# Kernel tuning notes

Hardware: AMD Instinct MI355X
Metric: run time of the kernel (lower is better)

Reference implementation:

```python
import jax, jax.numpy as jnp
import numpy as np

B, T, IN, H, OUT = 16384, 200, 9, 64, 3


def setup_inputs() -> dict:
    key = jax.random.key(0)
    ks = jax.random.split(key, 12)
    s_in, s_h = 1.0 / np.sqrt(H), 1.0 / np.sqrt(H)  # torch LSTMCell init scale = 1/sqrt(hidden)
    u = lambda k, shape: jax.random.uniform(k, shape, jnp.float32, -s_h, s_h)
    return {
        "x": jax.random.normal(ks[0], (B, T, IN), jnp.float32),
        "W_ih1": u(ks[1], (4 * H, IN)),
        "W_hh1": u(ks[2], (4 * H, H)),
        "b_ih1": u(ks[3], (4 * H,)),
        "b_hh1": u(ks[4], (4 * H,)),
        "W_ih2": u(ks[5], (4 * H, H)),
        "W_hh2": u(ks[6], (4 * H, H)),
        "b_ih2": u(ks[7], (4 * H,)),
        "b_hh2": u(ks[8], (4 * H,)),
        "W_out": u(ks[9], (OUT, H)),
        "b_out": u(ks[10], (OUT,)),
    }


def _lstm_cell(x, h, c, W_ih, W_hh, b_ih, b_hh):
    # PyTorch gate order: i, f, g, o
    gates = x @ W_ih.T + b_ih + h @ W_hh.T + b_hh  # [B, 4H]
    i, f, g, o = jnp.split(gates, 4, axis=-1)
    i, f, o = jax.nn.sigmoid(i), jax.nn.sigmoid(f), jax.nn.sigmoid(o)
    g = jnp.tanh(g)
    c_new = f * c + i * g
    h_new = o * jnp.tanh(c_new)
    return h_new, c_new


def reference(x, W_ih1, W_hh1, b_ih1, b_hh1, W_ih2, W_hh2, b_ih2, b_hh2, W_out, b_out):
    batch = x.shape[0]
    hdim = W_hh1.shape[1]
    zeros = jnp.zeros((batch, hdim), x.dtype)
    init = (zeros, zeros, zeros, zeros)  # h1, c1, h2, c2

    def step(carry, x_t):
        h1, c1, h2, c2 = carry
        h1, c1 = _lstm_cell(x_t, h1, c1, W_ih1, W_hh1, b_ih1, b_hh1)
        h2, c2 = _lstm_cell(h1, h2, c2, W_ih2, W_hh2, b_ih2, b_hh2)
        return (h1, c1, h2, c2), None

    (h1, c1, h2, c2), _ = jax.lax.scan(step, init, jnp.swapaxes(x, 0, 1))  # scan over time
    out = h2 @ W_out.T + b_out  # [B, OUT]
    return out[:, None, :]  # [B, 1, OUT]
```

## Files before the change

### kernel.cpp

```cpp
#include <hip/hip_runtime.h>
#include <hip/hip_bf16.h>


#define B_TOT   16384
#define T_STEPS 200
#define IN_DIM  9
#define HDIM    64

#define PK1_OFF 0
#define PK2_OFF 24576
#define BSUM_HALF_OFF 57344
#define PACK_W_TOT 57344
#define PACK_TOT (PACK_W_TOT + 512)

#define L2E     1.44269504089f
#define TWOL2E  2.88539008178f

typedef _Float16 half8  __attribute__((ext_vector_type(8)));
typedef _Float16 half4v __attribute__((ext_vector_type(4)));
typedef float    f32x4  __attribute__((ext_vector_type(4)));
typedef float    f4u    __attribute__((ext_vector_type(4), aligned(4)));

__global__ void pack_kernel(const float* __restrict__ Wih1, const float* __restrict__ Whh1,
                            const float* __restrict__ bih1, const float* __restrict__ bhh1,
                            const float* __restrict__ Wih2, const float* __restrict__ Whh2,
                            const float* __restrict__ bih2, const float* __restrict__ bhh2,
                            float* __restrict__ ws) {
    int e = blockIdx.x * 256 + threadIdx.x;
    if (e >= PACK_TOT) return;
    _Float16* wh = (_Float16*)ws;
    float* bptr = (float*)(wh + BSUM_HALF_OFF);
    auto gscale = [](int q) -> float {
        int gt = q >> 6;
        return (gt == 2) ? (-2.0f * L2E) : -L2E;
    };
    if (e < PK2_OFF) {
        int j = e & 7, lane = (e >> 3) & 63, nt = (e >> 9) & 15, c = e >> 13;
        int k = c * 32 + 4 * (lane >> 4) + (j & 3) + 16 * (j >> 2);
        int q = nt * 16 + (lane & 15);
        float v = 0.0f;
        if (k < 64)      v = Whh1[q * 64 + k];
        else if (k < 73) v = Wih1[q * 9 + (k - 64)];
        wh[e] = (_Float16)(v * gscale(q));
    } else if (e < PACK_W_TOT) {
        int e2 = e - PK2_OFF;
        int j = e2 & 7, lane = (e2 >> 3) & 63, nt = (e2 >> 9) & 15, c = e2 >> 13;
        int k = c * 32 + 4 * (lane >> 4) + (j & 3) + 16 * (j >> 2);
        int q = nt * 16 + (lane & 15);
        float v = (k < 64) ? Wih2[q * 64 + k] : Whh2[q * 64 + (k - 64)];
        wh[e] = (_Float16)(v * gscale(q));
    } else if (e < PACK_W_TOT + 256) {
        int q = e - PACK_W_TOT;
        bptr[q] = (bih1[q] + bhh1[q]) * gscale(q);
    } else {
        int q = e - PACK_W_TOT - 256;
        bptr[256 + q] = (bih2[q] + bhh2[q]) * gscale(q);
    }
}

__global__ __launch_bounds__(256, 2) void lstm_mfma(
    const float* __restrict__ x,
    const float* __restrict__ ws_f,
    const float* __restrict__ Wout,
    const float* __restrict__ bout,
    float* __restrict__ out)
{
    const int tid  = threadIdx.x;
    const int lane = tid & 63;
    const int w    = __builtin_amdgcn_readfirstlane(tid >> 6);
    const int l15  = lane & 15;
    const int l4   = lane >> 4;

    const _Float16* wh  = (const _Float16*)ws_f;
    const _Float16* pk1 = wh + PK1_OFF;
    const _Float16* pk2 = wh + PK2_OFF;
    const float* bsum   = (const float*)(wh + BSUM_HALF_OFF);

    __shared__ _Float16 h1P[2][16][72], h2P[2][16][72];
    __shared__ _Float16 h1Q[2][16][72], h2Q[2][16][72];
    __shared__ _Float16 xwP[2][8][4][16][4], xwQ[2][8][4][16][4];

    for (int i = tid; i < 2 * 16 * 72; i += 256) {
        (&h1P[0][0][0])[i] = (_Float16)0.0f; (&h2P[0][0][0])[i] = (_Float16)0.0f;
        (&h1Q[0][0][0])[i] = (_Float16)0.0f; (&h2Q[0][0][0])[i] = (_Float16)0.0f;
    }
    for (int i = tid; i < 2 * 8 * 4 * 16 * 4; i += 256) {
        (&xwP[0][0][0][0][0])[i] = (_Float16)0.0f;
        (&xwQ[0][0][0][0][0])[i] = (_Float16)0.0f;
    }

    const int bbase = blockIdx.x * 32;

    const int b_ = tid & 15, z_ = tid >> 4;
    const int s0_ = (z_ * 11) >> 5, q0_ = z_ - 3 * s0_;
    const bool act1 = (z_ < 8);
    const int pz1 = z_ + 16;
    const int s1_ = (pz1 * 11) >> 5, q1_ = pz1 - 3 * s1_;
    const float* xbP = x + (long)(bbase + b_) * (T_STEPS * IN_DIM);
    const float* xbQ = x + (long)(bbase + 16 + b_) * (T_STEPS * IN_DIM);

    f4u pfPA = {0.f,0.f,0.f,0.f}, pfPB = {0.f,0.f,0.f,0.f};
    f4u pfQA = {0.f,0.f,0.f,0.f}, pfQB = {0.f,0.f,0.f,0.f};

    auto fetch_t = [&](const float* xb, f4u& A, f4u& B, int wb) {
        int t0 = wb + s0_; if (t0 > T_STEPS - 1) t0 = T_STEPS - 1;
        const float* p0 = xb + t0 * IN_DIM + 4 * q0_;
        if (q0_ < 2) A = *(const f4u*)p0; else A[0] = p0[0];
        if (act1) {
            int t1 = wb + s1_; if (t1 > T_STEPS - 1) t1 = T_STEPS - 1;
            const float* p1 = xb + t1 * IN_DIM + 4 * q1_;
            if (q1_ < 2) B = *(const f4u*)p1; else B[0] = p1[0];
        }
    };
    auto store_t = [&](_Float16 (*xw)[8][4][16][4], f4u A, f4u B, int buf) {
        if (q0_ == 2) { A[1] = 0.f; A[2] = 0.f; A[3] = 0.f; }
        half4v hv;
        hv[0] = (_Float16)A[0]; hv[1] = (_Float16)A[1];
        hv[2] = (_Float16)A[2]; hv[3] = (_Float16)A[3];
        *(half4v*)&xw[buf][s0_][q0_][b_][0] = hv;
        if (act1) {
            if (q1_ == 2) { B[1] = 0.f; B[2] = 0.f; B[3] = 0.f; }
            half4v hw;
            hw[0] = (_Float16)B[0]; hw[1] = (_Float16)B[1];
            hw[2] = (_Float16)B[2]; hw[3] = (_Float16)B[3];
            *(half4v*)&xw[buf][s1_][q1_][b_][0] = hw;
        }
    };
    auto read_ax = [&](const _Float16 (*xw)[8][4][16][4], int tt) -> half8 {
        half4v xq = *(const half4v*)&xw[(tt >> 3) & 1][tt & 7][l4][l15][0];
        return __builtin_shufflevector(xq, xq, 0, 1, 2, 3, 0, 1, 2, 3);
    };

    half8 bw1_00, bw1_01, bw1_02, bw1_03;
    half8 bw1_10, bw1_11, bw1_12, bw1_13;
    half8 bw1_20, bw1_21, bw1_22, bw1_23;
    half8 bw2_00, bw2_01, bw2_02, bw2_03;
    half8 bw2_10, bw2_11, bw2_12, bw2_13;
    half8 bw2_20, bw2_21, bw2_22, bw2_23;
    half8 bw2_30, bw2_31, bw2_32, bw2_33;
    {
        #define LD1(c,g) *(const half8*)(pk1 + (((c * 16) + (w + 4 * g)) * 64 + lane) * 8)
        #define LD2(c,g) *(const half8*)(pk2 + (((c * 16) + (w + 4 * g)) * 64 + lane) * 8)
        bw1_00 = LD1(0,0); bw1_01 = LD1(0,1); bw1_02 = LD1(0,2); bw1_03 = LD1(0,3);
        bw1_10 = LD1(1,0); bw1_11 = LD1(1,1); bw1_12 = LD1(1,2); bw1_13 = LD1(1,3);
        bw1_20 = LD1(2,0); bw1_21 = LD1(2,1); bw1_22 = LD1(2,2); bw1_23 = LD1(2,3);
        bw2_00 = LD2(0,0); bw2_01 = LD2(0,1); bw2_02 = LD2(0,2); bw2_03 = LD2(0,3);
        bw2_10 = LD2(1,0); bw2_11 = LD2(1,1); bw2_12 = LD2(1,2); bw2_13 = LD2(1,3);
        bw2_20 = LD2(2,0); bw2_21 = LD2(2,1); bw2_22 = LD2(2,2); bw2_23 = LD2(2,3);
        bw2_30 = LD2(3,0); bw2_31 = LD2(3,1); bw2_32 = LD2(3,2); bw2_33 = LD2(3,3);
        #undef LD1
        #undef LD2
    }

    float bias1[4], bias2[4];
    #pragma unroll
    for (int g = 0; g < 4; ++g) {
        bias1[g] = bsum[(w + 4 * g) * 16 + l15];
        bias2[g] = bsum[256 + (w + 4 * g) * 16 + l15];
    }

    const int hpos = ((w >> 1) << 5) + 8 * (l15 >> 2) + (l15 & 3) + ((w & 1) << 2);

    f32x4 c1P = {0.f,0.f,0.f,0.f}, c2P = {0.f,0.f,0.f,0.f};
    f32x4 c1Q = {0.f,0.f,0.f,0.f}, c2Q = {0.f,0.f,0.f,0.f};

    auto cell_update = [&](f32x4* G, f32x4& cs, _Float16* hb) {
        float num[4], den[4], eo4[4], d2[4], hs4[4];
        #pragma unroll
        for (int r = 0; r < 4; ++r) {
            float ei = __builtin_amdgcn_exp2f(G[0][r]);
            float ef = __builtin_amdgcn_exp2f(G[1][r]);
            float eg = __builtin_amdgcn_exp2f(G[2][r]);
            eo4[r]   = __builtin_amdgcn_exp2f(G[3][r]);
            float ai = 1.0f + ei, af = 1.0f + ef, ag = 1.0f + eg;
            float gm = 1.0f - eg;
            float pp = ai * ag;
            num[r] = __builtin_fmaf(gm, af, cs[r] * pp);
            den[r] = af * pp;
        }
        float s01 = den[0] * den[1], s23 = den[2] * den[3];
        float Pinv = __builtin_amdgcn_rcpf(s01 * s23);
        float r01 = Pinv * s23, r23 = Pinv * s01;
        float inv[4] = {r01 * den[1], r01 * den[0], r23 * den[3], r23 * den[2]};
        #pragma unroll
        for (int r = 0; r < 4; ++r) {
            float cc = num[r] * inv[r];
            cs[r] = cc;
            float z  = cc * TWOL2E;
            int   zi = __float_as_int(z);
            float ec = __builtin_amdgcn_exp2f(__int_as_float(zi | (int)0x80000000));
            float tm = 1.0f - ec;
            d2[r] = (1.0f + eo4[r]) * (1.0f + ec);
            hs4[r] = __int_as_float(__float_as_int(tm) ^ (zi & (int)0x80000000));
        }
        float t01 = d2[0] * d2[1], t23 = d2[2] * d2[3];
        float Qinv = __builtin_amdgcn_rcpf(t01 * t23);
        float q01 = Qinv * t23, q23 = Qinv * t01;
        float jnv[4] = {q01 * d2[1], q01 * d2[0], q23 * d2[3], q23 * d2[2]};
        #pragma unroll
        for (int r = 0; r < 4; ++r)
            hb[(4 * l4 + r) * 72 + hpos] = (_Float16)(hs4[r] * jnv[r]);
    };

    auto initb = [&](f32x4* A, const float* b) {
        #pragma unroll
        for (int g = 0; g < 4; ++g) A[g] = (f32x4){b[g], b[g], b[g], b[g]};
    };
    auto L2C = [&](f32x4* D, half8 u0, half8 u1, half8 v0, half8 v1) {
        D[0] = __builtin_amdgcn_mfma_f32_16x16x32_f16(u0, bw2_00, D[0], 0, 0, 0);
        D[1] = __builtin_amdgcn_mfma_f32_16x16x32_f16(u0, bw2_01, D[1], 0, 0, 0);
        D[2] = __builtin_amdgcn_mfma_f32_16x16x32_f16(u0, bw2_02, D[2], 0, 0, 0);
        D[3] = __builtin_amdgcn_mfma_f32_16x16x32_f16(u0, bw2_03, D[3], 0, 0, 0);
        D[0] = __builtin_amdgcn_mfma_f32_16x16x32_f16(u1, bw2_10, D[0], 0, 0, 0);
        D[1] = __builtin_amdgcn_mfma_f32_16x16x32_f16(u1, bw2_11, D[1], 0, 0, 0);
        D[2] = __builtin_amdgcn_mfma_f32_16x16x32_f16(u1, bw2_12, D[2], 0, 0, 0);
        D[3] = __builtin_amdgcn_mfma_f32_16x16x32_f16(u1, bw2_13, D[3], 0, 0, 0);
        D[0] = __builtin_amdgcn_mfma_f32_16x16x32_f16(v0, bw2_20, D[0], 0, 0, 0);
        D[1] = __builtin_amdgcn_mfma_f32_16x16x32_f16(v0, bw2_21, D[1], 0, 0, 0);
        D[2] = __builtin_amdgcn_mfma_f32_16x16x32_f16(v0, bw2_22, D[2], 0, 0, 0);
        D[3] = __builtin_amdgcn_mfma_f32_16x16x32_f16(v0, bw2_23, D[3], 0, 0, 0);
        D[0] = __builtin_amdgcn_mfma_f32_16x16x32_f16(v1, bw2_30, D[0], 0, 0, 0);
        D[1] = __builtin_amdgcn_mfma_f32_16x16x32_f16(v1, bw2_31, D[1], 0, 0, 0);
        D[2] = __builtin_amdgcn_mfma_f32_16x16x32_f16(v1, bw2_32, D[2], 0, 0, 0);
        D[3] = __builtin_amdgcn_mfma_f32_16x16x32_f16(v1, bw2_33, D[3], 0, 0, 0);
    };
    auto L1C = [&](f32x4* C, half8 u0, half8 u1, half8 axm) {
        C[0] = __builtin_amdgcn_mfma_f32_16x16x32_f16(u0, bw1_00, C[0], 0, 0, 0);
        C[1] = __builtin_amdgcn_mfma_f32_16x16x32_f16(u0, bw1_01, C[1], 0, 0, 0);
        C[2] = __builtin_amdgcn_mfma_f32_16x16x32_f16(u0, bw1_02, C[2], 0, 0, 0);
        C[3] = __builtin_amdgcn_mfma_f32_16x16x32_f16(u0, bw1_03, C[3], 0, 0, 0);
        C[0] = __builtin_amdgcn_mfma_f32_16x16x32_f16(u1, bw1_10, C[0], 0, 0, 0);
        C[1] = __builtin_amdgcn_mfma_f32_16x16x32_f16(u1, bw1_11, C[1], 0, 0, 0);
        C[2] = __builtin_amdgcn_mfma_f32_16x16x32_f16(u1, bw1_12, C[2], 0, 0, 0);
        C[3] = __builtin_amdgcn_mfma_f32_16x16x32_f16(u1, bw1_13, C[3], 0, 0, 0);
        C[0] = __builtin_amdgcn_mfma_f32_16x16x32_f16(axm, bw1_20, C[0], 0, 0, 0);
        C[1] = __builtin_amdgcn_mfma_f32_16x16x32_f16(axm, bw1_21, C[1], 0, 0, 0);
        C[2] = __builtin_amdgcn_mfma_f32_16x16x32_f16(axm, bw1_22, C[2], 0, 0, 0);
        C[3] = __builtin_amdgcn_mfma_f32_16x16x32_f16(axm, bw1_23, C[3], 0, 0, 0);
    };

    #define PIN_ALL() do {                                                      \
        asm volatile("" :                                                       \
            "+v"(bw1_00), "+v"(bw1_01), "+v"(bw1_02), "+v"(bw1_03),             \
            "+v"(bw1_10), "+v"(bw1_11), "+v"(bw1_12), "+v"(bw1_13),             \
            "+v"(bw1_20), "+v"(bw1_21), "+v"(bw1_22), "+v"(bw1_23));            \
        asm volatile("" :                                                       \
            "+v"(bw2_00), "+v"(bw2_01), "+v"(bw2_02), "+v"(bw2_03),             \
            "+v"(bw2_10), "+v"(bw2_11), "+v"(bw2_12), "+v"(bw2_13),             \
            "+v"(bw2_20), "+v"(bw2_21), "+v"(bw2_22), "+v"(bw2_23),             \
            "+v"(bw2_30), "+v"(bw2_31), "+v"(bw2_32), "+v"(bw2_33),             \
            "+v"(bias1[0]), "+v"(bias1[1]), "+v"(bias1[2]), "+v"(bias1[3]),     \
            "+v"(bias2[0]), "+v"(bias2[1]), "+v"(bias2[2]), "+v"(bias2[3]));    \
    } while (0)

    fetch_t(xbP, pfPA, pfPB, 0);
    fetch_t(xbQ, pfQA, pfQB, 0);
    __syncthreads();
    store_t(xwP, pfPA, pfPB, 0);
    store_t(xwQ, pfQA, pfQB, 0);
    fetch_t(xbP, pfPA, pfPB, 8);
    fetch_t(xbQ, pfQA, pfQB, 8);
    __syncthreads();

    f32x4 CP[4], CQ[4];
    {
        half8 ax0 = read_ax(xwP, 0);
        initb(CP, bias1);
        CP[0] = __builtin_amdgcn_mfma_f32_16x16x32_f16(ax0, bw1_20, CP[0], 0, 0, 0);
        CP[1] = __builtin_amdgcn_mfma_f32_16x16x32_f16(ax0, bw1_21, CP[1], 0, 0, 0);
        CP[2] = __builtin_amdgcn_mfma_f32_16x16x32_f16(ax0, bw1_22, CP[2], 0, 0, 0);
        CP[3] = __builtin_amdgcn_mfma_f32_16x16x32_f16(ax0, bw1_23, CP[3], 0, 0, 0);
        half8 ax1 = read_ax(xwQ, 0);
        initb(CQ, bias1);
        CQ[0] = __builtin_amdgcn_mfma_f32_16x16x32_f16(ax1, bw1_20, CQ[0], 0, 0, 0);
        CQ[1] = __builtin_amdgcn_mfma_f32_16x16x32_f16(ax1, bw1_21, CQ[1], 0, 0, 0);
        CQ[2] = __builtin_amdgcn_mfma_f32_16x16x32_f16(ax1, bw1_22, CQ[2], 0, 0, 0);
        CQ[3] = __builtin_amdgcn_mfma_f32_16x16x32_f16(ax1, bw1_23, CQ[3], 0, 0, 0);
    }

    for (int t = 0; t < T_STEPS; t += 2) {
        PIN_ALL();
        cell_update(CP, c1P, &h1P[1][0][0]);
        cell_update(CQ, c1Q, &h1Q[1][0][0]);
        if ((t & 7) == 0) {
            int nb = ((t >> 3) + 1) & 1;
            store_t(xwP, pfPA, pfPB, nb);
            store_t(xwQ, pfQA, pfQB, nb);
            fetch_t(xbP, pfPA, pfPB, t + 16);
            fetch_t(xbQ, pfQA, pfQB, t + 16);
        }
        __syncthreads();
        __builtin_amdgcn_s_setprio(1);
        {
            half8 u0 = *(const half8*)&h1P[1][l15][ 0 + 8 * l4];
            half8 u1 = *(const half8*)&h1P[1][l15][32 + 8 * l4];
            half8 v0 = *(const half8*)&h2P[0][l15][ 0 + 8 * l4];
            half8 v1 = *(const half8*)&h2P[0][l15][32 + 8 * l4];
            half8 axm = read_ax(xwP, t + 1);
            f32x4 D[4]; initb(D, bias2);
            L2C(D, u0, u1, v0, v1);
            initb(CP, bias1);
            L1C(CP, u0, u1, axm);
            cell_update(D, c2P, &h2P[1][0][0]);
        }
        {
            half8 u0 = *(const half8*)&h1Q[1][l15][ 0 + 8 * l4];
            half8 u1 = *(const half8*)&h1Q[1][l15][32 + 8 * l4];
            half8 v0 = *(const half8*)&h2Q[0][l15][ 0 + 8 * l4];
            half8 v1 = *(const half8*)&h2Q[0][l15][32 + 8 * l4];
            half8 axm = read_ax(xwQ, t + 1);
            f32x4 D[4]; initb(D, bias2);
            L2C(D, u0, u1, v0, v1);
            initb(CQ, bias1);
            L1C(CQ, u0, u1, axm);
            cell_update(D, c2Q, &h2Q[1][0][0]);
        }
        __builtin_amdgcn_s_setprio(0);

        PIN_ALL();
        cell_update(CP, c1P, &h1P[0][0][0]);
        cell_update(CQ, c1Q, &h1Q[0][0][0]);
        __syncthreads();
        __builtin_amdgcn_s_setprio(1);
        {
            half8 u0 = *(const half8*)&h1P[0][l15][ 0 + 8 * l4];
            half8 u1 = *(const half8*)&h1P[0][l15][32 + 8 * l4];
            half8 v0 = *(const half8*)&h2P[1][l15][ 0 + 8 * l4];
            half8 v1 = *(const half8*)&h2P[1][l15][32 + 8 * l4];
            half8 axm = read_ax(xwP, t + 2);
            f32x4 D[4]; initb(D, bias2);
            L2C(D, u0, u1, v0, v1);
            initb(CP, bias1);
            L1C(CP, u0, u1, axm);
            cell_update(D, c2P, &h2P[0][0][0]);
        }
        {
            half8 u0 = *(const half8*)&h1Q[0][l15][ 0 + 8 * l4];
            half8 u1 = *(const half8*)&h1Q[0][l15][32 + 8 * l4];
            half8 v0 = *(const half8*)&h2Q[1][l15][ 0 + 8 * l4];
            half8 v1 = *(const half8*)&h2Q[1][l15][32 + 8 * l4];
            half8 axm = read_ax(xwQ, t + 2);
            f32x4 D[4]; initb(D, bias2);
            L2C(D, u0, u1, v0, v1);
            initb(CQ, bias1);
            L1C(CQ, u0, u1, axm);
            cell_update(D, c2Q, &h2Q[0][0][0]);
        }
        __builtin_amdgcn_s_setprio(0);
    }
    __syncthreads();

    if (tid < 96) {
        int bl = tid / 3, o = tid - bl * 3;
        const _Float16* src = (bl < 16) ? &h2P[0][bl][0] : &h2Q[0][bl - 16][0];
        float acc = bout[o];
        #pragma unroll 8
        for (int pos = 0; pos < HDIM; ++pos) {
            int sub = pos & 31;
            int j = (pos >> 5) * 32 + (((sub >> 2) & 1) << 4) + ((sub >> 3) << 2) + (sub & 3);
            acc = __builtin_fmaf(Wout[o * 64 + j], (float)src[pos], acc);
        }
        out[(bbase + bl) * 3 + o] = acc;
    }
    #undef PIN_ALL
}

extern "C" void kernel_launch(void* const* d_in, const int* in_sizes, int n_in,
                              void* d_out, int out_size, void* d_ws, size_t ws_size,
                              hipStream_t stream) {
    const float* x     = (const float*)d_in[0];
    const float* Wih1  = (const float*)d_in[1];
    const float* Whh1  = (const float*)d_in[2];
    const float* bih1  = (const float*)d_in[3];
    const float* bhh1  = (const float*)d_in[4];
    const float* Wih2  = (const float*)d_in[5];
    const float* Whh2  = (const float*)d_in[6];
    const float* bih2  = (const float*)d_in[7];
    const float* bhh2  = (const float*)d_in[8];
    const float* Wout  = (const float*)d_in[9];
    const float* bout  = (const float*)d_in[10];
    float* ws  = (float*)d_ws;
    float* out = (float*)d_out;

    pack_kernel<<<(PACK_TOT + 255) / 256, 256, 0, stream>>>(
        Wih1, Whh1, bih1, bhh1, Wih2, Whh2, bih2, bhh2, ws);

    lstm_mfma<<<B_TOT / 32, 256, 0, stream>>>(x, ws, Wout, bout, out);
}
```

Baseline: 557.4 us.

## Load x per step directly into registers instead of staging through LDS

Removes the shared-memory staging buffers for the input sequence, along with their cooperative fetch and store every eight steps. Each lane now prefetches its own x slice from global memory one step ahead and builds the MFMA A operand in registers. This drops LDS traffic and extra shuffle work, but adds a small global load on every step with only one step of latency hiding. The s_setprio hints around the MFMA phases are also removed, and the per-step body is refactored into a tile_phase helper.

```diff
diff --git a/kernel.cpp b/kernel.cpp
--- a/kernel.cpp
+++ b/kernel.cpp
@@ -17,7 +17,6 @@
 #define TWOL2E  2.88539008178f
 
 typedef _Float16 half8  __attribute__((ext_vector_type(8)));
-typedef _Float16 half4v __attribute__((ext_vector_type(4)));
 typedef float    f32x4  __attribute__((ext_vector_type(4)));
 typedef float    f4u    __attribute__((ext_vector_type(4), aligned(4)));
 
@@ -78,57 +77,30 @@
 
     __shared__ _Float16 h1P[2][16][72], h2P[2][16][72];
     __shared__ _Float16 h1Q[2][16][72], h2Q[2][16][72];
-    __shared__ _Float16 xwP[2][8][4][16][4], xwQ[2][8][4][16][4];
 
     for (int i = tid; i < 2 * 16 * 72; i += 256) {
         (&h1P[0][0][0])[i] = (_Float16)0.0f; (&h2P[0][0][0])[i] = (_Float16)0.0f;
         (&h1Q[0][0][0])[i] = (_Float16)0.0f; (&h2Q[0][0][0])[i] = (_Float16)0.0f;
     }
-    for (int i = tid; i < 2 * 8 * 4 * 16 * 4; i += 256) {
-        (&xwP[0][0][0][0][0])[i] = (_Float16)0.0f;
-        (&xwQ[0][0][0][0][0])[i] = (_Float16)0.0f;
-    }
 
     const int bbase = blockIdx.x * 32;
-
-    const int b_ = tid & 15, z_ = tid >> 4;
-    const int s0_ = (z_ * 11) >> 5, q0_ = z_ - 3 * s0_;
-    const bool act1 = (z_ < 8);
-    const int pz1 = z_ + 16;
-    const int s1_ = (pz1 * 11) >> 5, q1_ = pz1 - 3 * s1_;
-    const float* xbP = x + (long)(bbase + b_) * (T_STEPS * IN_DIM);
-    const float* xbQ = x + (long)(bbase + 16 + b_) * (T_STEPS * IN_DIM);
-
-    f4u pfPA = {0.f,0.f,0.f,0.f}, pfPB = {0.f,0.f,0.f,0.f};
-    f4u pfQA = {0.f,0.f,0.f,0.f}, pfQB = {0.f,0.f,0.f,0.f};
-
-    auto fetch_t = [&](const float* xb, f4u& A, f4u& B, int wb) {
-        int t0 = wb + s0_; if (t0 > T_STEPS - 1) t0 = T_STEPS - 1;
-        const float* p0 = xb + t0 * IN_DIM + 4 * q0_;
-        if (q0_ < 2) A = *(const f4u*)p0; else A[0] = p0[0];
-        if (act1) {
-            int t1 = wb + s1_; if (t1 > T_STEPS - 1) t1 = T_STEPS - 1;
-            const float* p1 = xb + t1 * IN_DIM + 4 * q1_;
-            if (q1_ < 2) B = *(const f4u*)p1; else B[0] = p1[0];
-        }
-    };
-    auto store_t = [&](_Float16 (*xw)[8][4][16][4], f4u A, f4u B, int buf) {
-        if (q0_ == 2) { A[1] = 0.f; A[2] = 0.f; A[3] = 0.f; }
-        half4v hv;
-        hv[0] = (_Float16)A[0]; hv[1] = (_Float16)A[1];
-        hv[2] = (_Float16)A[2]; hv[3] = (_Float16)A[3];
-        *(half4v*)&xw[buf][s0_][q0_][b_][0] = hv;
-        if (act1) {
-            if (q1_ == 2) { B[1] = 0.f; B[2] = 0.f; B[3] = 0.f; }
-            half4v hw;
-            hw[0] = (_Float16)B[0]; hw[1] = (_Float16)B[1];
-            hw[2] = (_Float16)B[2]; hw[3] = (_Float16)B[3];
-            *(half4v*)&xw[buf][s1_][q1_][b_][0] = hw;
-        }
-    };
-    auto read_ax = [&](const _Float16 (*xw)[8][4][16][4], int tt) -> half8 {
-        half4v xq = *(const half4v*)&xw[(tt >> 3) & 1][tt & 7][l4][l15][0];
-        return __builtin_shufflevector(xq, xq, 0, 1, 2, 3, 0, 1, 2, 3);
+    const float* xbP = x + (long)(bbase + l15) * (T_STEPS * IN_DIM);
+    const float* xbQ = x + (long)(bbase + 16 + l15) * (T_STEPS * IN_DIM);
+
+    f4u  cxP = {0.f,0.f,0.f,0.f}, cxQ = {0.f,0.f,0.f,0.f};
+    float cx8P = 0.0f, cx8Q = 0.0f;
+    auto prefetch_tile = [&](const float* xb, f4u& cx, float& cx8, int tt) {
+        const float* xp = xb + tt * IN_DIM;
+        if (l4 < 2)       cx  = *(const f4u*)(xp + 4 * l4);
+        else if (l4 == 2) cx8 = xp[8];
+    };
+    auto build_ax2 = [&](const f4u& cx, float cx8) -> half8 {
+        half8 ax;
+        float e0 = (l4 == 2) ? cx8 : cx[0];
+        ax[0] = (_Float16)e0;    ax[1] = (_Float16)cx[1];
+        ax[2] = (_Float16)cx[2]; ax[3] = (_Float16)cx[3];
+        ax[4] = ax[5] = ax[6] = ax[7] = (_Float16)0.0f;
+        return ax;
     };
 
     half8 bw1_00, bw1_01, bw1_02, bw1_03;
@@ -206,7 +178,15 @@
         #pragma unroll
         for (int g = 0; g < 4; ++g) A[g] = (f32x4){b[g], b[g], b[g], b[g]};
     };
-    auto L2C = [&](f32x4* D, half8 u0, half8 u1, half8 v0, half8 v1) {
+
+    auto tile_phase = [&](f32x4* Cacc, f32x4& cs2,
+                          const _Float16* h1w, const _Float16* h2r,
+                          _Float16* h2w, half8 axn) {
+        half8 u0 = *(const half8*)(h1w + l15 * 72 +  0 + 8 * l4);
+        half8 u1 = *(const half8*)(h1w + l15 * 72 + 32 + 8 * l4);
+        half8 v0 = *(const half8*)(h2r + l15 * 72 +  0 + 8 * l4);
+        half8 v1 = *(const half8*)(h2r + l15 * 72 + 32 + 8 * l4);
+        f32x4 D[4]; initb(D, bias2);
         D[0] = __builtin_amdgcn_mfma_f32_16x16x32_f16(u0, bw2_00, D[0], 0, 0, 0);
         D[1] = __builtin_amdgcn_mfma_f32_16x16x32_f16(u0, bw2_01, D[1], 0, 0, 0);
         D[2] = __builtin_amdgcn_mfma_f32_16x16x32_f16(u0, bw2_02, D[2], 0, 0, 0);
@@ -223,20 +203,20 @@
         D[1] = __builtin_amdgcn_mfma_f32_16x16x32_f16(v1, bw2_31, D[1], 0, 0, 0);
         D[2] = __builtin_amdgcn_mfma_f32_16x16x32_f16(v1, bw2_32, D[2], 0, 0, 0);
         D[3] = __builtin_amdgcn_mfma_f32_16x16x32_f16(v1, bw2_33, D[3], 0, 0, 0);
-    };
-    auto L1C = [&](f32x4* C, half8 u0, half8 u1, half8 axm) {
-        C[0] = __builtin_amdgcn_mfma_f32_16x16x32_f16(u0, bw1_00, C[0], 0, 0, 0);
-        C[1] = __builtin_amdgcn_mfma_f32_16x16x32_f16(u0, bw1_01, C[1], 0, 0, 0);
-        C[2] = __builtin_amdgcn_mfma_f32_16x16x32_f16(u0, bw1_02, C[2], 0, 0, 0);
-        C[3] = __builtin_amdgcn_mfma_f32_16x16x32_f16(u0, bw1_03, C[3], 0, 0, 0);
-        C[0] = __builtin_amdgcn_mfma_f32_16x16x32_f16(u1, bw1_10, C[0], 0, 0, 0);
-        C[1] = __builtin_amdgcn_mfma_f32_16x16x32_f16(u1, bw1_11, C[1], 0, 0, 0);
-        C[2] = __builtin_amdgcn_mfma_f32_16x16x32_f16(u1, bw1_12, C[2], 0, 0, 0);
-        C[3] = __builtin_amdgcn_mfma_f32_16x16x32_f16(u1, bw1_13, C[3], 0, 0, 0);
-        C[0] = __builtin_amdgcn_mfma_f32_16x16x32_f16(axm, bw1_20, C[0], 0, 0, 0);
-        C[1] = __builtin_amdgcn_mfma_f32_16x16x32_f16(axm, bw1_21, C[1], 0, 0, 0);
-        C[2] = __builtin_amdgcn_mfma_f32_16x16x32_f16(axm, bw1_22, C[2], 0, 0, 0);
-        C[3] = __builtin_amdgcn_mfma_f32_16x16x32_f16(axm, bw1_23, C[3], 0, 0, 0);
+        initb(Cacc, bias1);
+        Cacc[0] = __builtin_amdgcn_mfma_f32_16x16x32_f16(u0, bw1_00, Cacc[0], 0, 0, 0);
+        Cacc[1] = __builtin_amdgcn_mfma_f32_16x16x32_f16(u0, bw1_01, Cacc[1], 0, 0, 0);
+        Cacc[2] = __builtin_amdgcn_mfma_f32_16x16x32_f16(u0, bw1_02, Cacc[2], 0, 0, 0);
+        Cacc[3] = __builtin_amdgcn_mfma_f32_16x16x32_f16(u0, bw1_03, Cacc[3], 0, 0, 0);
+        Cacc[0] = __builtin_amdgcn_mfma_f32_16x16x32_f16(u1, bw1_10, Cacc[0], 0, 0, 0);
+        Cacc[1] = __builtin_amdgcn_mfma_f32_16x16x32_f16(u1, bw1_11, Cacc[1], 0, 0, 0);
+        Cacc[2] = __builtin_amdgcn_mfma_f32_16x16x32_f16(u1, bw1_12, Cacc[2], 0, 0, 0);
+        Cacc[3] = __builtin_amdgcn_mfma_f32_16x16x32_f16(u1, bw1_13, Cacc[3], 0, 0, 0);
+        Cacc[0] = __builtin_amdgcn_mfma_f32_16x16x32_f16(axn, bw1_20, Cacc[0], 0, 0, 0);
+        Cacc[1] = __builtin_amdgcn_mfma_f32_16x16x32_f16(axn, bw1_21, Cacc[1], 0, 0, 0);
+        Cacc[2] = __builtin_amdgcn_mfma_f32_16x16x32_f16(axn, bw1_22, Cacc[2], 0, 0, 0);
+        Cacc[3] = __builtin_amdgcn_mfma_f32_16x16x32_f16(axn, bw1_23, Cacc[3], 0, 0, 0);
+        cell_update(D, cs2, h2w);
     };
 
     #define PIN_ALL() do {                                                      \
@@ -253,100 +233,49 @@
             "+v"(bias2[0]), "+v"(bias2[1]), "+v"(bias2[2]), "+v"(bias2[3]));    \
     } while (0)
 
-    fetch_t(xbP, pfPA, pfPB, 0);
-    fetch_t(xbQ, pfQA, pfQB, 0);
-    __syncthreads();
-    store_t(xwP, pfPA, pfPB, 0);
-    store_t(xwQ, pfQA, pfQB, 0);
-    fetch_t(xbP, pfPA, pfPB, 8);
-    fetch_t(xbQ, pfQA, pfQB, 8);
-    __syncthreads();
-
+    prefetch_tile(xbP, cxP, cx8P, 0);
+    prefetch_tile(xbQ, cxQ, cx8Q, 0);
     f32x4 CP[4], CQ[4];
     {
-        half8 ax0 = read_ax(xwP, 0);
+        half8 ax0 = build_ax2(cxP, cx8P);
         initb(CP, bias1);
         CP[0] = __builtin_amdgcn_mfma_f32_16x16x32_f16(ax0, bw1_20, CP[0], 0, 0, 0);
         CP[1] = __builtin_amdgcn_mfma_f32_16x16x32_f16(ax0, bw1_21, CP[1], 0, 0, 0);
         CP[2] = __builtin_amdgcn_mfma_f32_16x16x32_f16(ax0, bw1_22, CP[2], 0, 0, 0);
         CP[3] = __builtin_amdgcn_mfma_f32_16x16x32_f16(ax0, bw1_23, CP[3], 0, 0, 0);
-        half8 ax1 = read_ax(xwQ, 0);
+        half8 ax1 = build_ax2(cxQ, cx8Q);
         initb(CQ, bias1);
         CQ[0] = __builtin_amdgcn_mfma_f32_16x16x32_f16(ax1, bw1_20, CQ[0], 0, 0, 0);
         CQ[1] = __builtin_amdgcn_mfma_f32_16x16x32_f16(ax1, bw1_21, CQ[1], 0, 0, 0);
         CQ[2] = __builtin_amdgcn_mfma_f32_16x16x32_f16(ax1, bw1_22, CQ[2], 0, 0, 0);
         CQ[3] = __builtin_amdgcn_mfma_f32_16x16x32_f16(ax1, bw1_23, CQ[3], 0, 0, 0);
     }
+    prefetch_tile(xbP, cxP, cx8P, 1);
+    prefetch_tile(xbQ, cxQ, cx8Q, 1);
+    __syncthreads();
 
     for (int t = 0; t < T_STEPS; t += 2) {
         PIN_ALL();
+        half8 axP = build_ax2(cxP, cx8P);
+        half8 axQ = build_ax2(cxQ, cx8Q);
+        prefetch_tile(xbP, cxP, cx8P, t + 2 < T_STEPS ? t + 2 : T_STEPS - 1);
+        prefetch_tile(xbQ, cxQ, cx8Q, t + 2 < T_STEPS ? t + 2 : T_STEPS - 1);
         cell_update(CP, c1P, &h1P[1][0][0]);
         cell_update(CQ, c1Q, &h1Q[1][0][0]);
-        if ((t & 7) == 0) {
-            int nb = ((t >> 3) + 1) & 1;
-            store_t(xwP, pfPA, pfPB, nb);
-            store_t(xwQ, pfQA, pfQB, nb);
-            fetch_t(xbP, pfPA, pfPB, t + 16);
-            fetch_t(xbQ, pfQA, pfQB, t + 16);
-        }
         __syncthreads();
-        __builtin_amdgcn_s_setprio(1);
-        {
-            half8 u0 = *(const half8*)&h1P[1][l15][ 0 + 8 * l4];
-            half8 u1 = *(const half8*)&h1P[1][l15][32 + 8 * l4];
-            half8 v0 = *(const half8*)&h2P[0][l15][ 0 + 8 * l4];
-            half8 v1 = *(const half8*)&h2P[0][l15][32 + 8 * l4];
-            half8 axm = read_ax(xwP, t + 1);
-            f32x4 D[4]; initb(D, bias2);
-            L2C(D, u0, u1, v0, v1);
-            initb(CP, bias1);
-            L1C(CP, u0, u1, axm);
-            cell_update(D, c2P, &h2P[1][0][0]);
-        }
-        {
-            half8 u0 = *(const half8*)&h1Q[1][l15][ 0 + 8 * l4];
-            half8 u1 = *(const half8*)&h1Q[1][l15][32 + 8 * l4];
-            half8 v0 = *(const half8*)&h2Q[0][l15][ 0 + 8 * l4];
-            half8 v1 = *(const half8*)&h2Q[0][l15][32 + 8 * l4];
-            half8 axm = read_ax(xwQ, t + 1);
-            f32x4 D[4]; initb(D, bias2);
-            L2C(D, u0, u1, v0, v1);
-            initb(CQ, bias1);
-            L1C(CQ, u0, u1, axm);
-            cell_update(D, c2Q, &h2Q[1][0][0]);
-        }
-        __builtin_amdgcn_s_setprio(0);
+        tile_phase(CP, c2P, &h1P[1][0][0], &h2P[0][0][0], &h2P[1][0][0], axP);
+        tile_phase(CQ, c2Q, &h1Q[1][0][0], &h2Q[0][0][0], &h2Q[1][0][0], axQ);
 
         PIN_ALL();
+        half8 bxP = build_ax2(cxP, cx8P);
+        half8 bxQ = build_ax2(cxQ, cx8Q);
+        prefetch_tile(xbP, cxP, cx8P, t + 3 < T_STEPS ? t + 3 : T_STEPS - 1);
+        prefetch_tile(xbQ, cxQ, cx8Q, t + 3 < T_STEPS ? t + 3 : T_STEPS - 1);
         cell_update(CP, c1P, &h1P[0][0][0]);
         cell_update(CQ, c1Q, &h1Q[0][0][0]);
         __syncthreads();
-        __builtin_amdgcn_s_setprio(1);
-        {
-            half8 u0 = *(const half8*)&h1P[0][l15][ 0 + 8 * l4];
-            half8 u1 = *(const half8*)&h1P[0][l15][32 + 8 * l4];
-            half8 v0 = *(const half8*)&h2P[1][l15][ 0 + 8 * l4];
-            half8 v1 = *(const half8*)&h2P[1][l15][32 + 8 * l4];
-            half8 axm = read_ax(xwP, t + 2);
-            f32x4 D[4]; initb(D, bias2);
-            L2C(D, u0, u1, v0, v1);
-            initb(CP, bias1);
-            L1C(CP, u0, u1, axm);
-            cell_update(D, c2P, &h2P[0][0][0]);
-        }
-        {
-            half8 u0 = *(const half8*)&h1Q[0][l15][ 0 + 8 * l4];
-            half8 u1 = *(const half8*)&h1Q[0][l15][32 + 8 * l4];
-            half8 v0 = *(const half8*)&h2Q[1][l15][ 0 + 8 * l4];
-            half8 v1 = *(const half8*)&h2Q[1][l15][32 + 8 * l4];
-            half8 axm = read_ax(xwQ, t + 2);
-            f32x4 D[4]; initb(D, bias2);
-            L2C(D, u0, u1, v0, v1);
-            initb(CQ, bias1);
-            L1C(CQ, u0, u1, axm);
-            cell_update(D, c2Q, &h2Q[0][0][0]);
-        }
-        __builtin_amdgcn_s_setprio(0);
+        tile_phase(CP, c2P, &h1P[0][0][0], &h2P[1][0][0], &h2P[0][0][0], bxP);
+        tile_phase(CQ, c2Q, &h1Q[0][0][0], &h2Q[1][0][0], &h2Q[0][0][0], bxQ);
     }
     __syncthreads();
 
```

Result: slower. 652.0 us (+17.0%).
